# Kernel optimization log

Hardware: AMD Instinct MI355X
Metric: run time of the kernel (lower is better)

## Reference

```python
import jax, jax.numpy as jnp
import numpy as np

N_LAYERS, B, S, D, H, DH = 4, 4, 512, 512, 8, 64
MEM, CMEM, RATIO, FFMUL, VOCAB, LLAT = 512, 128, 4, 4, 512, 256
KV = CMEM + MEM + S  # 1152


def layernorm(x, g, b, eps=1e-5):
    mu = x.mean(-1, keepdims=True)
    var = ((x - mu) ** 2).mean(-1, keepdims=True)
    return (x - mu) * jax.lax.rsqrt(var + eps) * g + b


def shift(x):
    # Music-Transformer skewing: x [..., i, j] -> relative-shifted [..., i, j]
    *lead, i, j = x.shape
    x = jnp.concatenate([x, jnp.zeros((*lead, i, i), x.dtype)], -1)
    l = i + j - 1
    x = x.reshape(*lead, i * (i + j))
    pad = (-x.shape[-1]) % l
    x = jnp.concatenate([x, jnp.zeros((*lead, pad), x.dtype)], -1)
    x = x.reshape(*lead, -1, l)
    return x[..., :i, i - 1:]


def full_attn(q, k, v, mask=None, pos_emb=None):
    dh = q.shape[-1]
    dots = jnp.einsum('bhid,bhjd->bhij', q, k) * (dh ** -0.5)
    if pos_emb is not None:
        pos_dots = jnp.einsum('bhid,hjd->bhij', q, pos_emb) * (dh ** 0.5)
        pos_dots = shift(pos_dots)[..., :dots.shape[-1]]
        dots = dots + pos_dots
    if mask is not None:
        dots = jnp.where(mask, dots, jnp.asarray(-1e9, dots.dtype))
    attn = jax.nn.softmax(dots, -1)
    return jnp.einsum('bhij,bhjd->bhid', attn, v), attn


def heads(x):
    b, n, _ = x.shape
    return x.reshape(b, n, H, DH).transpose(0, 2, 1, 3)


def mha(q_in, k_in, v_in, W, mask=None, pos_emb=None):
    # W: [4, D, D] (q, k, v, out), applied as x @ W
    q, k, v = heads(q_in @ W[0]), heads(k_in @ W[1]), heads(v_in @ W[2])
    x, w = full_attn(q, k, v, mask=mask, pos_emb=pos_emb)
    x = x.transpose(0, 2, 1, 3).reshape(q_in.shape[0], -1, D)
    return x @ W[3], w


def conv_compress(mem, w, b):
    # Conv1d(D, D, RATIO, stride=RATIO): kernel==stride -> block reshape
    Bb, L, _ = mem.shape
    m = mem.reshape(Bb, L // RATIO, RATIO, D)
    return jnp.einsum('blrd,odr->blo', m, w) + b


def forward(trg, trg_mask, src_mask, latent, mems, cmems, pos_emb, embed,
            W_self, ln1_g, ln1_b, conv_w, conv_b, W_src, ln2_g, ln2_b,
            w1, b1, w2, b2):
    x = jnp.take(embed, trg, axis=0)  # [B, S, D]
    tm = trg_mask[:, :, None] & trg_mask[:, None, :]  # [B, S, S]
    tm = jnp.pad(tm, ((0, 0), (0, 0), (CMEM + MEM, 0)), constant_values=True)[:, None]  # [B,1,S,KV]
    sm = src_mask[:, None]  # [B, 1, S, LLAT]
    sg = jax.lax.stop_gradient
    attn_loss = jnp.asarray(0.0, jnp.float32)
    for i in range(N_LAYERS):
        m, cm = mems[i], cmems[i]
        kv = jnp.concatenate([cm, m, x], 1)  # [B, KV, D]
        a, _ = mha(x, kv, kv, W_self[i], mask=tm, pos_emb=pos_emb)
        a = layernorm(a + x, ln1_g[i], ln1_b[i])
        old_mem = m[:, :S]
        new_cm = conv_compress(old_mem, conv_w[i], conv_b[i])  # [B, S//RATIO, D]
        x = a
        # reconstruction attention loss: detached h / weights / old_mem
        Wq, Wk, Wv = sg(W_self[i, 0]), sg(W_self[i, 1]), sg(W_self[i, 2])
        hs = sg(x)

        def rattn(mm):
            q, k, v = heads(hs @ Wq), heads(mm @ Wk), heads(mm @ Wv)
            return full_attn(q, k, v)[0]

        target = sg(rattn(sg(old_mem)))
        attn_loss = attn_loss + jnp.mean((rattn(new_cm) - target) ** 2)
        # cross attention to latent
        x, _ = mha(x, latent, latent, W_src[i], mask=sm)
        # residual pre-norm feed-forward (GELU, exact erf as nn.GELU)
        y = layernorm(x, ln2_g[i], ln2_b[i])
        x = x + jax.nn.gelu(y @ w1[i] + b1[i], approximate=False) @ w2[i] + b2[i]
    return x, attn_loss / N_LAYERS


def setup_inputs() -> dict:
    key = jax.random.key(0)
    ks = jax.random.split(key, 16)
    sc = 0.02
    return {
        'trg': jax.random.randint(ks[0], (B, S), 0, VOCAB, dtype=jnp.int32),
        'trg_mask': jnp.ones((B, S), dtype=bool),
        'src_mask': jnp.ones((B, S, LLAT), dtype=bool),
        'latent': jax.random.normal(ks[1], (B, LLAT, D), jnp.float32),
        'mems': jax.random.normal(ks[2], (N_LAYERS, B, MEM, D), jnp.float32) * sc,
        'cmems': jax.random.normal(ks[3], (N_LAYERS, B, CMEM, D), jnp.float32) * sc,
        'pos_emb': jax.random.normal(ks[4], (H, KV, DH), jnp.float32) * sc,
        'embed': jax.random.normal(ks[5], (VOCAB, D), jnp.float32) * sc,
        'W_self': jax.random.normal(ks[6], (N_LAYERS, 4, D, D), jnp.float32) * sc,
        'ln1_g': jnp.ones((N_LAYERS, D), jnp.float32),
        'ln1_b': jnp.zeros((N_LAYERS, D), jnp.float32),
        'conv_w': jax.random.normal(ks[7], (N_LAYERS, D, D, RATIO), jnp.float32) * sc,
        'conv_b': jnp.zeros((N_LAYERS, D), jnp.float32),
        'W_src': jax.random.normal(ks[8], (N_LAYERS, 4, D, D), jnp.float32) * sc,
        'ln2_g': jnp.ones((N_LAYERS, D), jnp.float32),
        'ln2_b': jnp.zeros((N_LAYERS, D), jnp.float32),
        'w1': jax.random.normal(ks[9], (N_LAYERS, D, D * FFMUL), jnp.float32) * sc,
        'b1': jnp.zeros((N_LAYERS, D * FFMUL), jnp.float32),
        'w2': jax.random.normal(ks[10], (N_LAYERS, D * FFMUL, D), jnp.float32) * sc,
        'b2': jnp.zeros((N_LAYERS, D), jnp.float32),
    }


def reference(trg, trg_mask, src_mask, latent, mems, cmems, pos_emb, embed,
              W_self, ln1_g, ln1_b, conv_w, conv_b, W_src, ln2_g, ln2_b,
              w1, b1, w2, b2):
    return forward(trg, trg_mask, src_mask, latent, mems, cmems, pos_emb, embed,
                   W_self, ln1_g, ln1_b, conv_w, conv_b, W_src, ln2_g, ln2_b,
                   w1, b1, w2, b2)
```

## Files before the change

kernel.cpp:

```cpp
#include <hip/hip_runtime.h>
#include <math.h>

typedef float floatx4 __attribute__((ext_vector_type(4)));
typedef __bf16 bf16x8 __attribute__((ext_vector_type(8)));
typedef unsigned short u16;

#define LDK 72

__device__ inline u16 to_bf16(float f) {
  union { float f; unsigned u; } v; v.f = f;
  unsigned u = v.u;
  u += 0x7FFFu + ((u >> 16) & 1u);
  return (u16)(u >> 16);
}
__device__ inline float bf2f(u16 h) {
  union { unsigned u; float f; } v; v.u = ((unsigned)h) << 16; return v.f;
}

__device__ inline void gload16(const void* g, void* l) {
  __builtin_amdgcn_global_load_lds(
      (const __attribute__((address_space(1))) unsigned int*)g,
      (__attribute__((address_space(3))) unsigned int*)l, 16, 0, 0);
}

struct GemmArgs {
  const void* A; const void* B; void* C;
  int lda, ldb, ldc, N, Kc;
  long sA1, sA2, sB1, sB2, sC1, sC2;
  float alpha;
  const float* bias;
  const float* res; int ldres;
  const float* aml;
  int amode;
  int cmode;
  int act;
  int smode;
  int bdiv, kparts;
  int gx, gy;
};

#define MAXG 6
struct GemmBatch {
  GemmArgs g[MAXG];
  int end[MAXG];
  int ng;
};

__global__ __launch_bounds__(256) void gemmb_k(GemmBatch gb) {
  int bid = blockIdx.x;
  int gi = 0;
  while (bid >= gb.end[gi]) ++gi;
  const GemmArgs g = gb.g[gi];
  int lb = bid - (gi ? gb.end[gi - 1] : 0);
  int bx = lb % g.gx;
  int rem = lb / g.gx;
  int by = rem % g.gy;
  int z = rem / g.gy;

  int kp = z % g.kparts;
  int zz = z / g.kparts;
  int zi = zz / g.bdiv, zj = zz % g.bdiv;
  long aoff = (long)zi * g.sA1 + (long)zj * g.sA2;
  long boff = (long)zi * g.sB1 + (long)zj * g.sB2;
  long coff = (long)zi * g.sC1 + (long)zj * g.sC2;
  const float* Af = (const float*)g.A + aoff;
  const u16* Ah = (const u16*)g.A + aoff;
  const u16* Bh = (const u16*)g.B + boff;

  int m0 = by * 64, n0 = bx * 64;
  __shared__ u16 As[64][64];
  __shared__ u16 Bs[64][64];
  char* Asb = (char*)&As[0][0];
  char* Bsb = (char*)&Bs[0][0];
  int tid = threadIdx.x;
  int wave = tid >> 6, lane = tid & 63;
  int wr = (wave >> 1) * 32, wc = (wave & 1) * 32;
  int lr = lane & 15, qrow = lane >> 4;

  unsigned o0 = wave * 1024u + lane * 16u;
  unsigned o1 = o0 + 4096u;
  int ga_r0 = o0 >> 7, ga_r1 = o1 >> 7;
  int ga_c0 = (int)(o0 & 127u) ^ ((ga_r0 & 7) << 4);
  int ga_c1 = (int)(o1 & 127u) ^ ((ga_r1 & 7) << 4);
  long ldaB = (long)g.lda * 2, ldbB = (long)g.ldb * 2;
  int r = tid >> 2, c16 = (tid & 3) << 4;
  int sw0 = (r << 7) + (((tid & 3) << 5) ^ ((r & 7) << 4));
  int sw1 = (r << 7) + ((((tid & 3) << 5) + 16) ^ ((r & 7) << 4));

  floatx4 acc[2][2];
#pragma unroll
  for (int i = 0; i < 2; ++i)
#pragma unroll
    for (int j = 0; j < 2; ++j)
#pragma unroll
      for (int rr = 0; rr < 4; ++rr) acc[i][j][rr] = 0.f;

  int kb0 = kp * g.Kc, kb1 = kb0 + g.Kc;
  for (int k0 = kb0; k0 < kb1; k0 += 64) {
    if (g.amode == 1) {
      const char* Ab = (const char*)Ah + ((long)m0 * g.lda + k0) * 2;
      gload16(Ab + ga_r0 * ldaB + ga_c0, Asb + wave * 1024);
      gload16(Ab + ga_r1 * ldaB + ga_c1, Asb + 4096 + wave * 1024);
    } else if (g.amode == 0) {
      const float* ap = Af + (long)(m0 + r) * g.lda + k0 + c16;
      float4 a0 = *(const float4*)ap, a1 = *(const float4*)(ap + 4);
      float4 a2 = *(const float4*)(ap + 8), a3 = *(const float4*)(ap + 12);
      union { u16 s[8]; uint4 v; } u0, u1;
      u0.s[0] = to_bf16(a0.x); u0.s[1] = to_bf16(a0.y); u0.s[2] = to_bf16(a0.z); u0.s[3] = to_bf16(a0.w);
      u0.s[4] = to_bf16(a1.x); u0.s[5] = to_bf16(a1.y); u0.s[6] = to_bf16(a1.z); u0.s[7] = to_bf16(a1.w);
      u1.s[0] = to_bf16(a2.x); u1.s[1] = to_bf16(a2.y); u1.s[2] = to_bf16(a2.z); u1.s[3] = to_bf16(a2.w);
      u1.s[4] = to_bf16(a3.x); u1.s[5] = to_bf16(a3.y); u1.s[6] = to_bf16(a3.z); u1.s[7] = to_bf16(a3.w);
      *(uint4*)(Asb + sw0) = u0.v; *(uint4*)(Asb + sw1) = u1.v;
    } else {
      int row = m0 + r;
      int k = k0 + c16;
      const float* mlp = g.aml + ((long)row * 8 + (k >> 6)) * 2;
      float m0v = mlp[0], l0v = mlp[1];
      float m1v = mlp[32768], l1v = mlp[32769];
      float mm = fmaxf(m0v, m1v);
      float w0 = __expf(m0v - mm), w1 = __expf(m1v - mm);
      float inv = 1.f / (w0 * l0v + w1 * l1v);
      w0 *= inv; w1 *= inv;
      const float* p0 = (const float*)g.A + (long)row * g.lda + k;
      const float* p1 = p0 + g.sA1;
      float4 x0 = *(const float4*)p0, x1 = *(const float4*)(p0 + 4);
      float4 x2 = *(const float4*)(p0 + 8), x3 = *(const float4*)(p0 + 12);
      float4 y0 = *(const float4*)p1, y1 = *(const float4*)(p1 + 4);
      float4 y2 = *(const float4*)(p1 + 8), y3 = *(const float4*)(p1 + 12);
      union { u16 s[8]; uint4 v; } u0, u1;
      u0.s[0] = to_bf16(w0 * x0.x + w1 * y0.x); u0.s[1] = to_bf16(w0 * x0.y + w1 * y0.y);
      u0.s[2] = to_bf16(w0 * x0.z + w1 * y0.z); u0.s[3] = to_bf16(w0 * x0.w + w1 * y0.w);
      u0.s[4] = to_bf16(w0 * x1.x + w1 * y1.x); u0.s[5] = to_bf16(w0 * x1.y + w1 * y1.y);
      u0.s[6] = to_bf16(w0 * x1.z + w1 * y1.z); u0.s[7] = to_bf16(w0 * x1.w + w1 * y1.w);
      u1.s[0] = to_bf16(w0 * x2.x + w1 * y2.x); u1.s[1] = to_bf16(w0 * x2.y + w1 * y2.y);
      u1.s[2] = to_bf16(w0 * x2.z + w1 * y2.z); u1.s[3] = to_bf16(w0 * x2.w + w1 * y2.w);
      u1.s[4] = to_bf16(w0 * x3.x + w1 * y3.x); u1.s[5] = to_bf16(w0 * x3.y + w1 * y3.y);
      u1.s[6] = to_bf16(w0 * x3.z + w1 * y3.z); u1.s[7] = to_bf16(w0 * x3.w + w1 * y3.w);
      *(uint4*)(Asb + sw0) = u0.v; *(uint4*)(Asb + sw1) = u1.v;
    }
    {
      const char* Bb = (const char*)Bh + ((long)n0 * g.ldb + k0) * 2;
      gload16(Bb + ga_r0 * ldbB + ga_c0, Bsb + wave * 1024);
      gload16(Bb + ga_r1 * ldbB + ga_c1, Bsb + 4096 + wave * 1024);
    }
    __syncthreads();
#pragma unroll
    for (int ks = 0; ks < 2; ++ks) {
      int xk = ((ks * 32 + qrow * 8) << 1) ^ ((lr & 7) << 4);
      int rA0 = wr + lr, rB0 = wc + lr;
      bf16x8 a0 = *(const bf16x8*)(Asb + (rA0 << 7) + xk);
      bf16x8 a1 = *(const bf16x8*)(Asb + ((rA0 + 16) << 7) + xk);
      bf16x8 b0 = *(const bf16x8*)(Bsb + (rB0 << 7) + xk);
      bf16x8 b1 = *(const bf16x8*)(Bsb + ((rB0 + 16) << 7) + xk);
      acc[0][0] = __builtin_amdgcn_mfma_f32_16x16x32_bf16(a0, b0, acc[0][0], 0, 0, 0);
      acc[0][1] = __builtin_amdgcn_mfma_f32_16x16x32_bf16(a0, b1, acc[0][1], 0, 0, 0);
      acc[1][0] = __builtin_amdgcn_mfma_f32_16x16x32_bf16(a1, b0, acc[1][0], 0, 0, 0);
      acc[1][1] = __builtin_amdgcn_mfma_f32_16x16x32_bf16(a1, b1, acc[1][1], 0, 0, 0);
    }
    __syncthreads();
  }

#pragma unroll
  for (int mt = 0; mt < 2; ++mt)
#pragma unroll
    for (int nt = 0; nt < 2; ++nt) {
      int row0 = m0 + wr + mt * 16 + qrow * 4;
      int col = n0 + wc + nt * 16 + lr;
      if (g.cmode == 2) {
        ushort4 o;
        o.x = to_bf16(acc[mt][nt][0] * g.alpha);
        o.y = to_bf16(acc[mt][nt][1] * g.alpha);
        o.z = to_bf16(acc[mt][nt][2] * g.alpha);
        o.w = to_bf16(acc[mt][nt][3] * g.alpha);
        *(ushort4*)((u16*)g.C + coff + (long)col * g.ldc + row0) = o;
      } else {
#pragma unroll
        for (int rr = 0; rr < 4; ++rr) {
          int row = row0 + rr;
          float v = acc[mt][nt][rr] * g.alpha;
          if (g.cmode == 3) {
            atomicAdd((float*)g.C + coff + (long)row * g.ldc + col, v);
          } else if (g.smode) {
            int oc = col + row - 511;
            if (oc >= 0) ((u16*)g.C + coff)[(long)row * g.ldc + oc] = to_bf16(v);
          } else {
            if (g.bias) v += g.bias[col];
            if (g.res) v += g.res[(long)row * g.ldres + col];
            if (g.act) v = 0.5f * v * (1.0f + erff(v * 0.70710678118654752f));
            if (g.cmode == 1) ((u16*)g.C + coff)[(long)row * g.ldc + col] = to_bf16(v);
            else ((float*)g.C + coff)[(long)row * g.ldc + col] = v;
          }
        }
      }
    }
}

struct FAttnArgs {
  const u16* Q; const u16* K; const u16* V; const u16* QP;
  void* O; float* Opart; float* ml;
  int L, nsplit; long sKb, sVb; int ldV;
  float scale; int obf16;
};

struct FBatch {
  FAttnArgs a[3];
  int zend[3];
  int nf;
};

__global__ __launch_bounds__(256) void fattnb_k(FBatch fb) {
  int zg = blockIdx.z;
  int fi = 0;
  while (zg >= fb.zend[fi]) ++fi;
  const FAttnArgs a = fb.a[fi];
  int zl = zg - (fi ? fb.zend[fi - 1] : 0);

  int qt = blockIdx.x, h = blockIdx.y;
  int b = zl / a.nsplit, sp = zl % a.nsplit;
  int Lc = a.L / a.nsplit, kt0 = sp * Lc, T = Lc >> 6;
  int tid = threadIdx.x, wave = tid >> 6, lane = tid & 63;
// ... 76 lines not shown
        qpr0 = *(const uint4*)(QPr + kt0 + (t + 1) * 64 + qc);
        qpr1 = *(const uint4*)(QPr + kt0 + (t + 1) * 64 + qc + 8);
      }
    } else {
#pragma unroll
      for (int nt = 0; nt < 4; ++nt)
#pragma unroll
        for (int rr = 0; rr < 4; ++rr) sacc[nt][rr] *= a.scale;
    }
#pragma unroll
    for (int rr = 0; rr < 4; ++rr) {
      float m = -1e30f;
#pragma unroll
      for (int nt = 0; nt < 4; ++nt) m = fmaxf(m, sacc[nt][rr]);
      for (int o = 8; o > 0; o >>= 1) m = fmaxf(m, __shfl_xor(m, o, 64));
      float mn = fmaxf(m_run[rr], m);
      float al = __expf(m_run[rr] - mn);
      m_run[rr] = mn;
      float s = 0.f;
#pragma unroll
      for (int nt = 0; nt < 4; ++nt) {
        float p = __expf(sacc[nt][rr] - mn);
        sacc[nt][rr] = p;
        s += p;
      }
      for (int o = 8; o > 0; o >>= 1) s += __shfl_xor(s, o, 64);
      l_run[rr] = l_run[rr] * al + s;
#pragma unroll
      for (int nt = 0; nt < 4; ++nt) oacc[nt][rr] *= al;
    }
#pragma unroll
    for (int nt = 0; nt < 4; ++nt) {
      Ps[wave][quad * 4 + 0][nt * 16 + lr] = to_bf16(sacc[nt][0]);
      Ps[wave][quad * 4 + 1][nt * 16 + lr] = to_bf16(sacc[nt][1]);
      Ps[wave][quad * 4 + 2][nt * 16 + lr] = to_bf16(sacc[nt][2]);
      Ps[wave][quad * 4 + 3][nt * 16 + lr] = to_bf16(sacc[nt][3]);
    }
#pragma unroll
    for (int ks = 0; ks < 2; ++ks) {
      int kq = ks * 32 + quad * 8;
      bf16x8 av = *(const bf16x8*)&Ps[wave][lr][kq];
#pragma unroll
      for (int nt = 0; nt < 4; ++nt) {
        bf16x8 bb = *(const bf16x8*)&Vs[cur][nt * 16 + lr][kq];
        oacc[nt] = __builtin_amdgcn_mfma_f32_16x16x32_bf16(av, bb, oacc[nt], 0, 0, 0);
      }
    }
    if (more) {
      *(uint4*)&Ks[cur ^ 1][r][c] = pk0; *(uint4*)&Ks[cur ^ 1][r][c + 8] = pk1;
      *(uint4*)&Vs[cur ^ 1][r][c] = pv0; *(uint4*)&Vs[cur ^ 1][r][c + 8] = pv1;
    }
  }
  if (a.nsplit == 1) {
    float inv[4];
#pragma unroll
    for (int rr = 0; rr < 4; ++rr) inv[rr] = 1.f / l_run[rr];
#pragma unroll
    for (int nt = 0; nt < 4; ++nt)
#pragma unroll
      for (int rr = 0; rr < 4; ++rr) {
        long row = b * 512 + qt * 64 + wave * 16 + quad * 4 + rr;
        float v = oacc[nt][rr] * inv[rr];
        if (a.obf16) ((u16*)a.O)[row * 512 + h * 64 + nt * 16 + lr] = to_bf16(v);
        else ((float*)a.O)[row * 512 + h * 64 + nt * 16 + lr] = v;
      }
  } else {
#pragma unroll
    for (int nt = 0; nt < 4; ++nt)
#pragma unroll
      for (int rr = 0; rr < 4; ++rr) {
        long row = b * 512 + qt * 64 + wave * 16 + quad * 4 + rr;
        a.Opart[((long)sp * 2048 + row) * 512 + h * 64 + nt * 16 + lr] = oacc[nt][rr];
      }
    if (lr == 0)
#pragma unroll
      for (int rr = 0; rr < 4; ++rr) {
        long row = b * 512 + qt * 64 + wave * 16 + quad * 4 + rr;
        long mi = (((long)sp * 2048 + row) * 8 + h) * 2;
        a.ml[mi] = m_run[rr]; a.ml[mi + 1] = l_run[rr];
      }
  }
}

__global__ __launch_bounds__(256) void embed_k(const int* __restrict__ trg,
                                               const float* __restrict__ embed,
                                               float* __restrict__ x) {
  int i = blockIdx.x * 256 + threadIdx.x;
  int row = i >> 9, d = i & 511;
  x[i] = embed[(long)trg[row] * 512 + d];
}

__global__ __launch_bounds__(256) void concat_kv_k(const float* __restrict__ cmem,
                                                   const float* __restrict__ mem,
                                                   const float* __restrict__ x,
                                                   u16* __restrict__ kv) {
  long i = (long)blockIdx.x * 256 + threadIdx.x;
  int d = i & 511;
  long t = (i >> 9) % 1152;
  long b = (i >> 9) / 1152;
  float v;
  if (t < 128) v = cmem[(b * 128 + t) * 512 + d];
  else if (t < 640) v = mem[(b * 512 + (t - 128)) * 512 + d];
  else v = x[(b * 512 + (t - 640)) * 512 + d];
  kv[i] = to_bf16(v);
}

__global__ __launch_bounds__(256) void layernorm_k(const float* __restrict__ X,
                                                   const float* __restrict__ g,
                                                   const float* __restrict__ b,
                                                   u16* __restrict__ Y) {
  long row = blockIdx.x;
  const float* x = X + row * 512;
  int tid = threadIdx.x;
  float v0 = x[tid], v1 = x[tid + 256];
  __shared__ float red[256];
  red[tid] = v0 + v1; __syncthreads();
  for (int o = 128; o > 0; o >>= 1) { if (tid < o) red[tid] += red[tid + o]; __syncthreads(); }
  float mu = red[0] * (1.f / 512.f);
  __syncthreads();
  float d0 = v0 - mu, d1 = v1 - mu;
  red[tid] = d0 * d0 + d1 * d1; __syncthreads();
  for (int o = 128; o > 0; o >>= 1) { if (tid < o) red[tid] += red[tid + o]; __syncthreads(); }
  float rstd = rsqrtf(red[0] * (1.f / 512.f) + 1e-5f);
  Y[row * 512 + tid] = to_bf16(d0 * rstd * g[tid] + b[tid]);
  Y[row * 512 + tid + 256] = to_bf16(d1 * rstd * g[tid + 256] + b[tid + 256]);
}

__global__ __launch_bounds__(256) void preset_k(float* __restrict__ C,
                                                const float* __restrict__ res,
                                                const float* __restrict__ bias, int nmask) {
  long i = (long)blockIdx.x * 256 + threadIdx.x;
  float v = 0.f;
  if (res) v += res[i];
  if (bias) v += bias[i & nmask];
  C[i] = v;
}

__global__ __launch_bounds__(256) void loss2_k(const float* __restrict__ ocm,
                                               const float* __restrict__ Opart,
                                               const float* __restrict__ ml,
                                               float* __restrict__ acc) {
  float s = 0.f;
  for (long i = (long)blockIdx.x * 256 + threadIdx.x; i < 1048576; i += 256L * 128) {
    int row = (int)(i >> 9), col = (int)(i & 511), h = col >> 6;
    const float* mlp = ml + ((long)row * 8 + h) * 2;
    float m0v = mlp[0], l0v = mlp[1];
    float m1v = mlp[32768], l1v = mlp[32769];
    float mm = fmaxf(m0v, m1v);
    float w0 = __expf(m0v - mm), w1 = __expf(m1v - mm);
    float ov = (w0 * Opart[i] + w1 * Opart[1048576 + i]) / (w0 * l0v + w1 * l1v);
    float d = ocm[i] - ov; s += d * d;
  }
  for (int o = 32; o > 0; o >>= 1) s += __shfl_xor(s, o, 64);
  __shared__ float red[4];
  if ((threadIdx.x & 63) == 0) red[threadIdx.x >> 6] = s;
  __syncthreads();
  if (threadIdx.x == 0) atomicAdd(acc, red[0] + red[1] + red[2] + red[3]);
}

__global__ __launch_bounds__(256) void transpose_bf16_k(const float* __restrict__ in,
                                                        u16* __restrict__ out, int K, int N) {
  long z = blockIdx.z;
  in += z * (long)K * N; out += z * (long)K * N;
  __shared__ float t[32][33];
  int n0 = blockIdx.x * 32, k0 = blockIdx.y * 32;
  int tx = threadIdx.x, ty = threadIdx.y;
  for (int j = 0; j < 32; j += 8) t[ty + j][tx] = in[(long)(k0 + ty + j) * N + n0 + tx];
  __syncthreads();
  for (int j = 0; j < 32; j += 8) out[(long)(n0 + ty + j) * K + k0 + tx] = to_bf16(t[tx][ty + j]);
}

__global__ __launch_bounds__(256) void convw_k(const float* __restrict__ in,
                                               u16* __restrict__ out) {
  int i = blockIdx.x * 256 + threadIdx.x;
  long z = blockIdx.z;
  int o = i >> 11, k = i & 2047;
  int r = k >> 9, d = k & 511;
  out[z * 1048576 + i] = to_bf16(in[z * 1048576 + o * 2048 + d * 4 + r]);
}

__global__ __launch_bounds__(256) void cvt_bf16_k(const float* __restrict__ in,
                                                  u16* __restrict__ out, int n) {
  int i = blockIdx.x * 256 + threadIdx.x;
  if (i < n) out[i] = to_bf16(in[i]);
}

__global__ __launch_bounds__(256) void finalize_k(const float* __restrict__ x,
                                                  const float* __restrict__ loss,
                                                  float* __restrict__ out) {
  long i = (long)blockIdx.x * 256 + threadIdx.x;
  if (i < 1048576) out[i] = x[i];
  else if (i == 1048576) out[i] = loss[0] * (1.f / (1048576.f * 4.f));
}

extern "C" void kernel_launch(void* const* d_in, const int* in_sizes, int n_in,
                              void* d_out, int out_size, void* d_ws, size_t ws_size,
                              hipStream_t stream) {
  (void)in_sizes; (void)n_in; (void)out_size;
  const int* trg = (const int*)d_in[0];
  const float* latent = (const float*)d_in[3];
  const float* mems = (const float*)d_in[4];
  const float* cmems = (const float*)d_in[5];
  const float* pos_emb = (const float*)d_in[6];
  const float* embed = (const float*)d_in[7];
  const float* W_self = (const float*)d_in[8];
  const float* ln1_g = (const float*)d_in[9];
  const float* ln1_b = (const float*)d_in[10];
  const float* conv_w = (const float*)d_in[11];
  const float* conv_b = (const float*)d_in[12];
  const float* W_src = (const float*)d_in[13];
  const float* ln2_g = (const float*)d_in[14];
  const float* ln2_b = (const float*)d_in[15];
  const float* w1 = (const float*)d_in[16];
  const float* b1 = (const float*)d_in[17];
  const float* w2 = (const float*)d_in[18];
  const float* b2 = (const float*)d_in[19];

  float* ws = (float*)d_ws;
  long off = 0;
  auto alloc = [&](long n) { float* p = ws + off; off += (n + 63) & ~63L; return p; };
  float* x    = alloc(1048576);
  float* t0   = alloc(1048576);
  float* t1   = alloc(1048576);
  float* ncm  = alloc(262144);
  float* ocm  = alloc(1048576);
  float* Opart= alloc(2097152);
  u16* h1   = (u16*)Opart;
  float* mlb  = alloc(65536);
  float* Opart2 = alloc(2097152);
  float* mlb2 = alloc(65536);
  u16* qb   = (u16*)alloc(524288);
  u16* qc   = (u16*)alloc(524288);
  u16* xa   = (u16*)alloc(524288);
  u16* t1h  = (u16*)alloc(524288);
  u16* kvcat= (u16*)alloc(1179648);
  u16* kbuf = (u16*)alloc(1179648);
  u16* vbuf = (u16*)alloc(1179648);
  u16* kmem = (u16*)alloc(524288);
  u16* vmem = (u16*)alloc(524288);
  u16* kcm  = (u16*)alloc(131072);
  u16* vcm  = (u16*)alloc(131072);
  u16* klat = (u16*)alloc(262144);
  u16* vlat = (u16*)alloc(262144);
  u16* SQP  = (u16*)alloc(9437184);
  u16* wts  = (u16*)alloc(2097152);
  u16* wsr  = (u16*)alloc(2097152);
  u16* w1t  = (u16*)alloc(2097152);
  u16* w2t  = (u16*)alloc(2097152);
  u16* cwt  = (u16*)alloc(2097152);
  u16* post = (u16*)alloc(294912);
  float* lossacc = alloc(64);
  if ((size_t)off * 4 > ws_size) return;

  hipMemsetAsync(lossacc, 0, 4, stream);
  hipMemsetAsync(SQP, 0, 37748736, stream);
  embed_k<<<4096, 256, 0, stream>>>(trg, embed, x);
  transpose_bf16_k<<<dim3(16, 16, 16), dim3(32, 8), 0, stream>>>(W_self, wts, 512, 512);
  transpose_bf16_k<<<dim3(16, 16, 16), dim3(32, 8), 0, stream>>>(W_src, wsr, 512, 512);
  transpose_bf16_k<<<dim3(64, 16, 4), dim3(32, 8), 0, stream>>>(w1, w1t, 512, 2048);
  transpose_bf16_k<<<dim3(16, 64, 4), dim3(32, 8), 0, stream>>>(w2, w2t, 2048, 512);
  convw_k<<<dim3(4096, 1, 4), 256, 0, stream>>>(conv_w, cwt);
  cvt_bf16_k<<<2304, 256, 0, stream>>>(pos_emb, post, 589824);

  auto ga = []() { GemmArgs g; g.alpha = 1.f; g.bias = nullptr; g.res = nullptr; g.ldres = 512;
                   g.aml = nullptr;
                   g.amode = 0; g.cmode = 0; g.act = 0; g.smode = 0; g.bdiv = 1; g.kparts = 1;
                   g.sA1 = g.sA2 = g.sB1 = g.sB2 = g.sC1 = g.sC2 = 0; g.N = 0;
                   g.gx = g.gy = 1; return g; };
  GemmBatch GB; GB.ng = 0; int gtot = 0;
  auto badd = [&](GemmArgs g, int gx, int gy, int gz) {
    g.gx = gx; g.gy = gy;
    GB.g[GB.ng] = g; gtot += gx * gy * gz; GB.end[GB.ng] = gtot; GB.ng++;
  };
  auto brun = [&]() {
    gemmb_k<<<dim3(gtot), 256, 0, stream>>>(GB);
    GB.ng = 0; gtot = 0;
  };
  auto run1 = [&](GemmArgs g, int gx, int gy, int gz) { badd(g, gx, gy, gz); brun(); };

  FBatch FB; FB.nf = 0; int ztot = 0;
  auto fadd = [&](const u16* Q, const u16* K, const u16* V, const u16* QP, void* O,
                  int L, int nsplit, long sKb, long sVb, int ldV, int obf16,
                  float* Op, float* ml) {
    FAttnArgs a; a.Q = Q; a.K = K; a.V = V; a.QP = QP; a.O = O;
    a.Opart = Op; a.ml = ml;
    a.L = L; a.nsplit = nsplit; a.sKb = sKb; a.sVb = sVb; a.ldV = ldV;
    a.scale = 0.125f; a.obf16 = obf16;
    FB.a[FB.nf] = a; ztot += 4 * nsplit; FB.zend[FB.nf] = ztot; FB.nf++;
  };
  auto frun = [&]() {
    fattnb_k<<<dim3(8, 8, ztot), 256, 0, stream>>>(FB);
    FB.nf = 0; ztot = 0;
  };

  for (int l = 0; l < 4; ++l) {
    const u16* Wt0 = wts + (l * 4 + 0) * 262144;
    const u16* Wt1 = wts + (l * 4 + 1) * 262144;
    const u16* Wt2 = wts + (l * 4 + 2) * 262144;
    const u16* Wt3 = wts + (l * 4 + 3) * 262144;
    const u16* Ws0 = wsr + (l * 4 + 0) * 262144;
    const u16* Ws1 = wsr + (l * 4 + 1) * 262144;
    const u16* Ws2 = wsr + (l * 4 + 2) * 262144;
    const u16* Ws3 = wsr + (l * 4 + 3) * 262144;
    const float* mem_l = mems + (long)l * 1048576;
    const float* cmem_l = cmems + (long)l * 262144;

    concat_kv_k<<<9216, 256, 0, stream>>>(cmem_l, mem_l, x, kvcat);
    preset_k<<<1024, 256, 0, stream>>>(ncm, nullptr, conv_b + l * 512, 511);
    { GemmArgs g = ga(); g.A = x; g.lda = 512; g.B = Wt0; g.ldb = 512; g.C = qb; g.ldc = 512;
      g.cmode = 1; g.Kc = 512; badd(g, 8, 32, 1); }
    { GemmArgs g = ga(); g.A = mem_l; g.lda = 2048; g.B = cwt + (long)l * 1048576; g.ldb = 2048;
      g.C = ncm; g.ldc = 512; g.cmode = 3; g.kparts = 8; g.Kc = 256; badd(g, 8, 8, 8); }
    { GemmArgs g = ga(); g.A = mem_l; g.lda = 512; g.B = Wt1; g.ldb = 512;
      g.C = kmem; g.ldc = 512; g.cmode = 1; g.Kc = 512; badd(g, 8, 32, 1); }
    { GemmArgs g = ga(); g.A = mem_l; g.lda = 512; g.B = Wt2; g.ldb = 512;
      g.C = vmem; g.ldc = 2048; g.cmode = 2; g.Kc = 512; badd(g, 8, 32, 1); }
    { GemmArgs g = ga(); g.A = latent; g.lda = 512; g.B = Ws1; g.ldb = 512;
      g.C = klat; g.ldc = 512; g.cmode = 1; g.Kc = 512; badd(g, 8, 16, 1); }
    { GemmArgs g = ga(); g.A = latent; g.lda = 512; g.B = Ws2; g.ldb = 512;
      g.C = vlat; g.ldc = 1024; g.cmode = 2; g.Kc = 512; badd(g, 8, 16, 1); }
    brun();

    { GemmArgs g = ga(); g.A = kvcat; g.amode = 1; g.lda = 512; g.B = Wt1; g.ldb = 512;
      g.C = kbuf; g.ldc = 512; g.cmode = 1; g.Kc = 512; badd(g, 8, 72, 1); }
    { GemmArgs g = ga(); g.A = kvcat; g.amode = 1; g.lda = 512; g.sA1 = 589824; g.B = Wt2; g.ldb = 512;
      g.C = vbuf; g.ldc = 1152; g.sC1 = 589824; g.cmode = 2; g.Kc = 512; badd(g, 8, 18, 4); }
    { GemmArgs g = ga(); g.A = ncm; g.lda = 512; g.B = Wt1; g.ldb = 512;
      g.C = kcm; g.ldc = 512; g.cmode = 1; g.Kc = 512; badd(g, 8, 8, 1); }
    { GemmArgs g = ga(); g.A = ncm; g.lda = 512; g.B = Wt2; g.ldb = 512;
      g.C = vcm; g.ldc = 512; g.cmode = 2; g.Kc = 512; badd(g, 8, 8, 1); }
    { GemmArgs g = ga(); g.A = qb; g.amode = 1; g.lda = 512; g.sA1 = 262144; g.sA2 = 64;
      g.B = post; g.ldb = 64; g.sB1 = 0; g.sB2 = 73728;
      g.C = SQP; g.ldc = 1152; g.sC1 = 4718592; g.sC2 = 589824;
      g.smode = 1; g.alpha = 8.f; g.bdiv = 8; g.Kc = 64; badd(g, 18, 8, 32); }
    brun();

    fadd(qb, kbuf, vbuf, SQP, nullptr, 1152, 2, 589824, 589824, 1152, 1, Opart, mlb);
    frun();
    { GemmArgs g = ga(); g.A = Opart; g.amode = 2; g.aml = mlb; g.lda = 512; g.sA1 = 1048576;
      g.B = Wt3; g.ldb = 512; g.C = t1; g.ldc = 512; g.res = x; g.Kc = 512; run1(g, 8, 32, 1); }
    layernorm_k<<<2048, 256, 0, stream>>>(t1, ln1_g + l * 512, ln1_b + l * 512, xa);

    { GemmArgs g = ga(); g.A = xa; g.amode = 1; g.lda = 512; g.B = Wt0; g.ldb = 512;
      g.C = qb; g.ldc = 512; g.cmode = 1; g.Kc = 512; badd(g, 8, 32, 1); }
    { GemmArgs g = ga(); g.A = xa; g.amode = 1; g.lda = 512; g.B = Ws0; g.ldb = 512;
      g.C = qc; g.ldc = 512; g.cmode = 1; g.Kc = 512; badd(g, 8, 32, 1); }
    brun();

    fadd(qb, kcm, vcm, nullptr, ocm, 128, 1, 65536, 128, 512, 0, Opart, mlb);
    fadd(qb, kmem, vmem, nullptr, nullptr, 512, 2, 262144, 512, 2048, 0, Opart, mlb);
    fadd(qc, klat, vlat, nullptr, nullptr, 256, 2, 131072, 256, 1024, 1, Opart2, mlb2);
    frun();
    loss2_k<<<128, 256, 0, stream>>>(ocm, Opart, mlb, lossacc);

    { GemmArgs g = ga(); g.A = Opart2; g.amode = 2; g.aml = mlb2; g.lda = 512; g.sA1 = 1048576;
      g.B = Ws3; g.ldb = 512; g.C = t0; g.ldc = 512; g.Kc = 512; run1(g, 8, 32, 1); }
    layernorm_k<<<2048, 256, 0, stream>>>(t0, ln2_g + l * 512, ln2_b + l * 512, t1h);

    { GemmArgs g = ga(); g.A = t1h; g.amode = 1; g.lda = 512; g.B = w1t + (long)l * 1048576; g.ldb = 512;
      g.C = h1; g.ldc = 2048; g.cmode = 1; g.bias = b1 + l * 2048; g.act = 1; g.Kc = 512;
      run1(g, 32, 32, 1); }
    preset_k<<<4096, 256, 0, stream>>>(x, t0, b2 + l * 512, 511);
    { GemmArgs g = ga(); g.A = h1; g.amode = 1; g.lda = 2048; g.B = w2t + (long)l * 1048576; g.ldb = 2048;
      g.C = x; g.ldc = 512; g.cmode = 3; g.kparts = 4; g.Kc = 512; run1(g, 8, 32, 4); }
  }
  finalize_k<<<4097, 256, 0, stream>>>(x, lossacc, (float*)d_out);
}
```

Baseline: 1.161 ms.

## Batch prep kernels, hoist layer-invariant projections, and fold elementwise ops into grouped GEMM launches

All preprocessing kernels (embedding, weight transposes, conv weight reorder, pos_emb conversion, bias preset, memsets) are merged into one batched prep kernel. Latent K/V projections, memory compression and compressed-memory K/V for all layers are hoisted out of the layer loop and computed once. The per-layer bf16 concat buffer is removed by projecting cmem, mem and x directly into kbuf/vbuf. Memory K/V is reused from kbuf/vbuf, and the attention split count goes to 3 with a generalized merge. The loss and residual-preset kernels are folded into the batched GEMM launch as special modes. The aim is fewer launches and less redundant projection work, at the cost of more workspace and a more complex dispatch.

```diff
diff --git a/kernel.cpp b/kernel.cpp
--- a/kernel.cpp
+++ b/kernel.cpp
@@ -39,7 +39,7 @@
   int gx, gy;
 };
 
-#define MAXG 6
+#define MAXG 10
 struct GemmBatch {
   GemmArgs g[MAXG];
   int end[MAXG];
@@ -52,6 +52,42 @@
   while (bid >= gb.end[gi]) ++gi;
   const GemmArgs g = gb.g[gi];
   int lb = bid - (gi ? gb.end[gi - 1] : 0);
+  int tid = threadIdx.x;
+
+  if (g.amode == 8) {
+    long i = (long)lb * 1024 + tid * 4;
+    const float* bs = g.bias;
+    int bi = (int)(i & 511);
+    float4 r = *(const float4*)(g.res + i);
+    float4 v;
+    v.x = r.x + bs[bi]; v.y = r.y + bs[bi + 1];
+    v.z = r.z + bs[bi + 2]; v.w = r.w + bs[bi + 3];
+    *(float4*)((float*)g.C + i) = v;
+    return;
+  }
+  if (g.amode == 9) {
+    const float* oc = (const float*)g.A;
+    const float* Op = (const float*)g.B;
+    const float* ml = g.aml;
+    float s = 0.f;
+    for (long i = (long)lb * 256 + tid; i < 1048576; i += 256L * g.gx) {
+      int row = (int)(i >> 9), col = (int)(i & 511), h = col >> 6;
+      const float* mlp = ml + ((long)row * 8 + h) * 2;
+      float m0v = mlp[0], l0v = mlp[1];
+      float m1v = mlp[32768], l1v = mlp[32769];
+      float mm = fmaxf(m0v, m1v);
+      float w0 = __expf(m0v - mm), w1 = __expf(m1v - mm);
+      float ov = (w0 * Op[i] + w1 * Op[1048576 + i]) / (w0 * l0v + w1 * l1v);
+      float d = oc[i] - ov; s += d * d;
+    }
+    for (int o = 32; o > 0; o >>= 1) s += __shfl_xor(s, o, 64);
+    __shared__ float red[4];
+    if ((tid & 63) == 0) red[tid >> 6] = s;
+    __syncthreads();
+    if (tid == 0) atomicAdd((float*)g.C, red[0] + red[1] + red[2] + red[3]);
+    return;
+  }
+
   int bx = lb % g.gx;
   int rem = lb / g.gx;
   int by = rem % g.gy;
@@ -72,7 +108,6 @@
   __shared__ u16 Bs[64][64];
   char* Asb = (char*)&As[0][0];
   char* Bsb = (char*)&Bs[0][0];
-  int tid = threadIdx.x;
   int wave = tid >> 6, lane = tid & 63;
   int wr = (wave >> 1) * 32, wc = (wave & 1) * 32;
   int lr = lane & 15, qrow = lane >> 4;
@@ -114,28 +149,38 @@
     } else {
       int row = m0 + r;
       int k = k0 + c16;
+      int ns = g.N;
       const float* mlp = g.aml + ((long)row * 8 + (k >> 6)) * 2;
-      float m0v = mlp[0], l0v = mlp[1];
-      float m1v = mlp[32768], l1v = mlp[32769];
-      float mm = fmaxf(m0v, m1v);
-      float w0 = __expf(m0v - mm), w1 = __expf(m1v - mm);
-      float inv = 1.f / (w0 * l0v + w1 * l1v);
-      w0 *= inv; w1 *= inv;
+      float mm = -1e30f;
+#pragma unroll 3
+      for (int s = 0; s < 3; ++s)
+        if (s < ns) mm = fmaxf(mm, mlp[s * 32768]);
+      float wgt[3]; float den = 0.f;
+#pragma unroll 3
+      for (int s = 0; s < 3; ++s)
+        if (s < ns) { wgt[s] = __expf(mlp[s * 32768] - mm); den += wgt[s] * mlp[s * 32768 + 1]; }
+      float inv = 1.f / den;
+      float a16[16];
+#pragma unroll
+      for (int j = 0; j < 16; ++j) a16[j] = 0.f;
       const float* p0 = (const float*)g.A + (long)row * g.lda + k;
-      const float* p1 = p0 + g.sA1;
-      float4 x0 = *(const float4*)p0, x1 = *(const float4*)(p0 + 4);
-      float4 x2 = *(const float4*)(p0 + 8), x3 = *(const float4*)(p0 + 12);
-      float4 y0 = *(const float4*)p1, y1 = *(const float4*)(p1 + 4);
-      float4 y2 = *(const float4*)(p1 + 8), y3 = *(const float4*)(p1 + 12);
+#pragma unroll 3
+      for (int s = 0; s < 3; ++s)
+        if (s < ns) {
+          float w = wgt[s] * inv;
+          const float* p = p0 + (long)s * g.sA1;
+#pragma unroll
+          for (int j = 0; j < 4; ++j) {
+            float4 xx = *(const float4*)(p + j * 4);
+            a16[j * 4 + 0] += w * xx.x; a16[j * 4 + 1] += w * xx.y;
+            a16[j * 4 + 2] += w * xx.z; a16[j * 4 + 3] += w * xx.w;
+          }
+        }
       union { u16 s[8]; uint4 v; } u0, u1;
-      u0.s[0] = to_bf16(w0 * x0.x + w1 * y0.x); u0.s[1] = to_bf16(w0 * x0.y + w1 * y0.y);
-      u0.s[2] = to_bf16(w0 * x0.z + w1 * y0.z); u0.s[3] = to_bf16(w0 * x0.w + w1 * y0.w);
-      u0.s[4] = to_bf16(w0 * x1.x + w1 * y1.x); u0.s[5] = to_bf16(w0 * x1.y + w1 * y1.y);
-      u0.s[6] = to_bf16(w0 * x1.z + w1 * y1.z); u0.s[7] = to_bf16(w0 * x1.w + w1 * y1.w);
-      u1.s[0] = to_bf16(w0 * x2.x + w1 * y2.x); u1.s[1] = to_bf16(w0 * x2.y + w1 * y2.y);
-      u1.s[2] = to_bf16(w0 * x2.z + w1 * y2.z); u1.s[3] = to_bf16(w0 * x2.w + w1 * y2.w);
-      u1.s[4] = to_bf16(w0 * x3.x + w1 * y3.x); u1.s[5] = to_bf16(w0 * x3.y + w1 * y3.y);
-      u1.s[6] = to_bf16(w0 * x3.z + w1 * y3.z); u1.s[7] = to_bf16(w0 * x3.w + w1 * y3.w);
+#pragma unroll
+      for (int j = 0; j < 8; ++j) u0.s[j] = to_bf16(a16[j]);
+#pragma unroll
+      for (int j = 0; j < 8; ++j) u1.s[j] = to_bf16(a16[8 + j]);
       *(uint4*)(Asb + sw0) = u0.v; *(uint4*)(Asb + sw1) = u1.v;
     }
     {
@@ -378,27 +423,45 @@
   }
 }
 
-__global__ __launch_bounds__(256) void embed_k(const int* __restrict__ trg,
-                                               const float* __restrict__ embed,
-                                               float* __restrict__ x) {
-  int i = blockIdx.x * 256 + threadIdx.x;
-  int row = i >> 9, d = i & 511;
-  x[i] = embed[(long)trg[row] * 512 + d];
-}
-
-__global__ __launch_bounds__(256) void concat_kv_k(const float* __restrict__ cmem,
-                                                   const float* __restrict__ mem,
-                                                   const float* __restrict__ x,
-                                                   u16* __restrict__ kv) {
-  long i = (long)blockIdx.x * 256 + threadIdx.x;
-  int d = i & 511;
-  long t = (i >> 9) % 1152;
-  long b = (i >> 9) / 1152;
-  float v;
-  if (t < 128) v = cmem[(b * 128 + t) * 512 + d];
-  else if (t < 640) v = mem[(b * 512 + (t - 128)) * 512 + d];
-  else v = x[(b * 512 + (t - 640)) * 512 + d];
-  kv[i] = to_bf16(v);
+struct PrepArgs { const void* a; const void* b; void* c; int mode, p0, p1, gx, gy; };
+struct PrepBatch { PrepArgs p[10]; int end[10]; int np; };
+
+__global__ __launch_bounds__(256) void prep_k(PrepBatch pb) {
+  int bid = blockIdx.x, gi = 0;
+  while (bid >= pb.end[gi]) ++gi;
+  PrepArgs p = pb.p[gi];
+  int lb = bid - (gi ? pb.end[gi - 1] : 0);
+  int tid = threadIdx.x;
+  __shared__ float t[32][33];
+  if (p.mode == 0) {
+    int i = lb * 256 + tid;
+    int row = i >> 9, d = i & 511;
+    ((float*)p.c)[i] = ((const float*)p.a)[(long)((const int*)p.b)[row] * 512 + d];
+  } else if (p.mode == 1) {
+    int K = p.p0, N = p.p1;
+    int bx = lb % p.gx, by = (lb / p.gx) % p.gy, z = lb / (p.gx * p.gy);
+    const float* in = (const float*)p.a + (long)z * K * N;
+    u16* out = (u16*)p.c + (long)z * K * N;
+    int n0 = bx * 32, k0 = by * 32;
+    int tx = tid & 31, ty = tid >> 5;
+    for (int j = 0; j < 32; j += 8) t[ty + j][tx] = in[(long)(k0 + ty + j) * N + n0 + tx];
+    __syncthreads();
+    for (int j = 0; j < 32; j += 8) out[(long)(n0 + ty + j) * K + k0 + tx] = to_bf16(t[tx][ty + j]);
+  } else if (p.mode == 2) {
+    int z = lb >> 12; int i = (lb & 4095) * 256 + tid;
+    int o = i >> 11, k = i & 2047, r2 = k >> 9, d = k & 511;
+    ((u16*)p.c)[(long)z * 1048576 + i] =
+        to_bf16(((const float*)p.a)[(long)z * 1048576 + o * 2048 + d * 4 + r2]);
+  } else if (p.mode == 3) {
+    int i = lb * 256 + tid;
+    if (i < p.p0) ((u16*)p.c)[i] = to_bf16(((const float*)p.a)[i]);
+  } else if (p.mode == 4) {
+    int i = lb * 256 + tid;
+    ((float*)p.c)[i] = ((const float*)p.a)[((i >> 18) << 9) + (i & 511)];
+  } else {
+    int i = lb * 256 + tid;
+    if (i < p.p0) { uint4 z4 = {0, 0, 0, 0}; ((uint4*)p.c)[i] = z4; }
+  }
 }
 
 __global__ __launch_bounds__(256) void layernorm_k(const float* __restrict__ X,
@@ -420,65 +483,6 @@
   float rstd = rsqrtf(red[0] * (1.f / 512.f) + 1e-5f);
   Y[row * 512 + tid] = to_bf16(d0 * rstd * g[tid] + b[tid]);
   Y[row * 512 + tid + 256] = to_bf16(d1 * rstd * g[tid + 256] + b[tid + 256]);
-}
-
-__global__ __launch_bounds__(256) void preset_k(float* __restrict__ C,
-                                                const float* __restrict__ res,
-                                                const float* __restrict__ bias, int nmask) {
-  long i = (long)blockIdx.x * 256 + threadIdx.x;
-  float v = 0.f;
-  if (res) v += res[i];
-  if (bias) v += bias[i & nmask];
-  C[i] = v;
-}
-
-__global__ __launch_bounds__(256) void loss2_k(const float* __restrict__ ocm,
-                                               const float* __restrict__ Opart,
-                                               const float* __restrict__ ml,
-                                               float* __restrict__ acc) {
-  float s = 0.f;
-  for (long i = (long)blockIdx.x * 256 + threadIdx.x; i < 1048576; i += 256L * 128) {
-    int row = (int)(i >> 9), col = (int)(i & 511), h = col >> 6;
-    const float* mlp = ml + ((long)row * 8 + h) * 2;
-    float m0v = mlp[0], l0v = mlp[1];
-    float m1v = mlp[32768], l1v = mlp[32769];
-    float mm = fmaxf(m0v, m1v);
-    float w0 = __expf(m0v - mm), w1 = __expf(m1v - mm);
-    float ov = (w0 * Opart[i] + w1 * Opart[1048576 + i]) / (w0 * l0v + w1 * l1v);
-    float d = ocm[i] - ov; s += d * d;
-  }
-  for (int o = 32; o > 0; o >>= 1) s += __shfl_xor(s, o, 64);
-  __shared__ float red[4];
-  if ((threadIdx.x & 63) == 0) red[threadIdx.x >> 6] = s;
-  __syncthreads();
-  if (threadIdx.x == 0) atomicAdd(acc, red[0] + red[1] + red[2] + red[3]);
-}
-
-__global__ __launch_bounds__(256) void transpose_bf16_k(const float* __restrict__ in,
-                                                        u16* __restrict__ out, int K, int N) {
-  long z = blockIdx.z;
-  in += z * (long)K * N; out += z * (long)K * N;
-  __shared__ float t[32][33];
-  int n0 = blockIdx.x * 32, k0 = blockIdx.y * 32;
-  int tx = threadIdx.x, ty = threadIdx.y;
-  for (int j = 0; j < 32; j += 8) t[ty + j][tx] = in[(long)(k0 + ty + j) * N + n0 + tx];
-  __syncthreads();
-  for (int j = 0; j < 32; j += 8) out[(long)(n0 + ty + j) * K + k0 + tx] = to_bf16(t[tx][ty + j]);
-}
-
-__global__ __launch_bounds__(256) void convw_k(const float* __restrict__ in,
-                                               u16* __restrict__ out) {
-  int i = blockIdx.x * 256 + threadIdx.x;
-  long z = blockIdx.z;
-  int o = i >> 11, k = i & 2047;
-  int r = k >> 9, d = k & 511;
-  out[z * 1048576 + i] = to_bf16(in[z * 1048576 + o * 2048 + d * 4 + r]);
-}
-
-__global__ __launch_bounds__(256) void cvt_bf16_k(const float* __restrict__ in,
-                                                  u16* __restrict__ out, int n) {
-  int i = blockIdx.x * 256 + threadIdx.x;
-  if (i < n) out[i] = to_bf16(in[i]);
 }
 
 __global__ __launch_bounds__(256) void finalize_k(const float* __restrict__ x,
@@ -518,26 +522,23 @@
   float* x    = alloc(1048576);
   float* t0   = alloc(1048576);
   float* t1   = alloc(1048576);
-  float* ncm  = alloc(262144);
   float* ocm  = alloc(1048576);
-  float* Opart= alloc(2097152);
-  u16* h1   = (u16*)Opart;
-  float* mlb  = alloc(65536);
+  float* Opart= alloc(3145728);
+  float* mlb  = alloc(98304);
   float* Opart2 = alloc(2097152);
+  u16* h1   = (u16*)Opart2;
   float* mlb2 = alloc(65536);
   u16* qb   = (u16*)alloc(524288);
   u16* qc   = (u16*)alloc(524288);
   u16* xa   = (u16*)alloc(524288);
   u16* t1h  = (u16*)alloc(524288);
-  u16* kvcat= (u16*)alloc(1179648);
   u16* kbuf = (u16*)alloc(1179648);
   u16* vbuf = (u16*)alloc(1179648);
-  u16* kmem = (u16*)alloc(524288);
-  u16* vmem = (u16*)alloc(524288);
-  u16* kcm  = (u16*)alloc(131072);
-  u16* vcm  = (u16*)alloc(131072);
-  u16* klat = (u16*)alloc(262144);
-  u16* vlat = (u16*)alloc(262144);
+  u16* kcm4 = (u16*)alloc(524288);
+  u16* vcm4 = (u16*)alloc(524288);
+  u16* klat4= (u16*)alloc(1048576);
+  u16* vlat4= (u16*)alloc(1048576);
+  float* ncm4 = alloc(1048576);
   u16* SQP  = (u16*)alloc(9437184);
   u16* wts  = (u16*)alloc(2097152);
   u16* wsr  = (u16*)alloc(2097152);
@@ -548,15 +549,24 @@
   float* lossacc = alloc(64);
   if ((size_t)off * 4 > ws_size) return;
 
-  hipMemsetAsync(lossacc, 0, 4, stream);
-  hipMemsetAsync(SQP, 0, 37748736, stream);
-  embed_k<<<4096, 256, 0, stream>>>(trg, embed, x);
-  transpose_bf16_k<<<dim3(16, 16, 16), dim3(32, 8), 0, stream>>>(W_self, wts, 512, 512);
-  transpose_bf16_k<<<dim3(16, 16, 16), dim3(32, 8), 0, stream>>>(W_src, wsr, 512, 512);
-  transpose_bf16_k<<<dim3(64, 16, 4), dim3(32, 8), 0, stream>>>(w1, w1t, 512, 2048);
-  transpose_bf16_k<<<dim3(16, 64, 4), dim3(32, 8), 0, stream>>>(w2, w2t, 2048, 512);
-  convw_k<<<dim3(4096, 1, 4), 256, 0, stream>>>(conv_w, cwt);
-  cvt_bf16_k<<<2304, 256, 0, stream>>>(pos_emb, post, 589824);
+  PrepBatch PB; PB.np = 0; int ptot = 0;
+  auto padd = [&](int mode, const void* a, const void* b, void* c,
+                  int p0, int p1, int gx, int gy, int blocks) {
+    PrepArgs pa; pa.a = a; pa.b = b; pa.c = c; pa.mode = mode;
+    pa.p0 = p0; pa.p1 = p1; pa.gx = gx; pa.gy = gy;
+    PB.p[PB.np] = pa; ptot += blocks; PB.end[PB.np] = ptot; PB.np++;
+  };
+  padd(0, embed, trg, x, 0, 0, 0, 0, 4096);
+  padd(1, W_self, nullptr, wts, 512, 512, 16, 16, 4096);
+  padd(1, W_src, nullptr, wsr, 512, 512, 16, 16, 4096);
+  padd(1, w1, nullptr, w1t, 512, 2048, 64, 16, 4096);
+  padd(1, w2, nullptr, w2t, 2048, 512, 16, 64, 4096);
+  padd(2, conv_w, nullptr, cwt, 0, 0, 0, 0, 16384);
+  padd(3, pos_emb, nullptr, post, 589824, 0, 0, 0, 2304);
+  padd(4, conv_b, nullptr, ncm4, 0, 0, 0, 0, 4096);
+  padd(5, nullptr, nullptr, SQP, 2359296, 0, 0, 0, 9216);
+  padd(5, nullptr, nullptr, lossacc, 1, 0, 0, 0, 1);
+  prep_k<<<dim3(ptot), 256, 0, stream>>>(PB);
 
   auto ga = []() { GemmArgs g; g.alpha = 1.f; g.bias = nullptr; g.res = nullptr; g.ldres = 512;
                    g.aml = nullptr;
@@ -589,52 +599,70 @@
     FB.nf = 0; ztot = 0;
   };
 
+  { GemmArgs g = ga(); g.A = latent; g.lda = 512; g.B = wsr + 262144; g.ldb = 512;
+    g.sB1 = 1048576; g.C = klat4; g.ldc = 512; g.sC1 = 524288; g.cmode = 1; g.Kc = 512;
+    badd(g, 8, 16, 4); }
+  { GemmArgs g = ga(); g.A = latent; g.lda = 512; g.B = wsr + 2 * 262144; g.ldb = 512;
+    g.sB1 = 1048576; g.C = vlat4; g.ldc = 1024; g.sC1 = 524288; g.cmode = 2; g.Kc = 512;
+    badd(g, 8, 16, 4); }
+  { GemmArgs g = ga(); g.A = mems; g.lda = 2048; g.sA1 = 1048576;
+    g.B = cwt; g.ldb = 2048; g.sB1 = 1048576;
+    g.C = ncm4; g.ldc = 512; g.sC1 = 262144; g.cmode = 3; g.kparts = 8; g.Kc = 256;
+    badd(g, 8, 8, 32); }
+  brun();
+
   for (int l = 0; l < 4; ++l) {
     const u16* Wt0 = wts + (l * 4 + 0) * 262144;
     const u16* Wt1 = wts + (l * 4 + 1) * 262144;
     const u16* Wt2 = wts + (l * 4 + 2) * 262144;
     const u16* Wt3 = wts + (l * 4 + 3) * 262144;
     const u16* Ws0 = wsr + (l * 4 + 0) * 262144;
-    const u16* Ws1 = wsr + (l * 4 + 1) * 262144;
-    const u16* Ws2 = wsr + (l * 4 + 2) * 262144;
     const u16* Ws3 = wsr + (l * 4 + 3) * 262144;
     const float* mem_l = mems + (long)l * 1048576;
     const float* cmem_l = cmems + (long)l * 262144;
-
-    concat_kv_k<<<9216, 256, 0, stream>>>(cmem_l, mem_l, x, kvcat);
-    preset_k<<<1024, 256, 0, stream>>>(ncm, nullptr, conv_b + l * 512, 511);
+    const u16* kcm_l = kcm4 + (long)l * 262144;
+    const u16* vcm_l = vcm4 + (long)l * 262144;
+    const u16* klat_l = klat4 + (long)l * 524288;
+    const u16* vlat_l = vlat4 + (long)l * 524288;
+
     { GemmArgs g = ga(); g.A = x; g.lda = 512; g.B = Wt0; g.ldb = 512; g.C = qb; g.ldc = 512;
       g.cmode = 1; g.Kc = 512; badd(g, 8, 32, 1); }
-    { GemmArgs g = ga(); g.A = mem_l; g.lda = 2048; g.B = cwt + (long)l * 1048576; g.ldb = 2048;
-      g.C = ncm; g.ldc = 512; g.cmode = 3; g.kparts = 8; g.Kc = 256; badd(g, 8, 8, 8); }
-    { GemmArgs g = ga(); g.A = mem_l; g.lda = 512; g.B = Wt1; g.ldb = 512;
-      g.C = kmem; g.ldc = 512; g.cmode = 1; g.Kc = 512; badd(g, 8, 32, 1); }
-    { GemmArgs g = ga(); g.A = mem_l; g.lda = 512; g.B = Wt2; g.ldb = 512;
-      g.C = vmem; g.ldc = 2048; g.cmode = 2; g.Kc = 512; badd(g, 8, 32, 1); }
-    { GemmArgs g = ga(); g.A = latent; g.lda = 512; g.B = Ws1; g.ldb = 512;
-      g.C = klat; g.ldc = 512; g.cmode = 1; g.Kc = 512; badd(g, 8, 16, 1); }
-    { GemmArgs g = ga(); g.A = latent; g.lda = 512; g.B = Ws2; g.ldb = 512;
-      g.C = vlat; g.ldc = 1024; g.cmode = 2; g.Kc = 512; badd(g, 8, 16, 1); }
+    { GemmArgs g = ga(); g.A = cmem_l; g.lda = 512; g.sA1 = 65536; g.B = Wt1; g.ldb = 512;
+      g.C = kbuf; g.ldc = 512; g.sC1 = 589824; g.cmode = 1; g.Kc = 512; badd(g, 8, 2, 4); }
+    { GemmArgs g = ga(); g.A = mem_l; g.lda = 512; g.sA1 = 262144; g.B = Wt1; g.ldb = 512;
+      g.C = kbuf + 128 * 512; g.ldc = 512; g.sC1 = 589824; g.cmode = 1; g.Kc = 512;
+      badd(g, 8, 8, 4); }
+    { GemmArgs g = ga(); g.A = x; g.lda = 512; g.sA1 = 262144; g.B = Wt1; g.ldb = 512;
+      g.C = kbuf + 640 * 512; g.ldc = 512; g.sC1 = 589824; g.cmode = 1; g.Kc = 512;
+      badd(g, 8, 8, 4); }
+    { GemmArgs g = ga(); g.A = cmem_l; g.lda = 512; g.sA1 = 65536; g.B = Wt2; g.ldb = 512;
+      g.C = vbuf; g.ldc = 1152; g.sC1 = 589824; g.cmode = 2; g.Kc = 512; badd(g, 8, 2, 4); }
+    { GemmArgs g = ga(); g.A = mem_l; g.lda = 512; g.sA1 = 262144; g.B = Wt2; g.ldb = 512;
+      g.C = vbuf + 128; g.ldc = 1152; g.sC1 = 589824; g.cmode = 2; g.Kc = 512;
+      badd(g, 8, 8, 4); }
+    { GemmArgs g = ga(); g.A = x; g.lda = 512; g.sA1 = 262144; g.B = Wt2; g.ldb = 512;
+      g.C = vbuf + 640; g.ldc = 1152; g.sC1 = 589824; g.cmode = 2; g.Kc = 512;
+      badd(g, 8, 8, 4); }
+    if (l == 0) {
+      { GemmArgs g = ga(); g.A = ncm4; g.lda = 512; g.sA1 = 262144; g.B = wts + 262144;
+        g.ldb = 512; g.sB1 = 1048576; g.C = kcm4; g.ldc = 512; g.sC1 = 262144;
+        g.cmode = 1; g.Kc = 512; badd(g, 8, 8, 4); }
+      { GemmArgs g = ga(); g.A = ncm4; g.lda = 512; g.sA1 = 262144; g.B = wts + 2 * 262144;
+        g.ldb = 512; g.sB1 = 1048576; g.C = vcm4; g.ldc = 512; g.sC1 = 262144;
+        g.cmode = 2; g.Kc = 512; badd(g, 8, 8, 4); }
+    }
     brun();
 
-    { GemmArgs g = ga(); g.A = kvcat; g.amode = 1; g.lda = 512; g.B = Wt1; g.ldb = 512;
-      g.C = kbuf; g.ldc = 512; g.cmode = 1; g.Kc = 512; badd(g, 8, 72, 1); }
-    { GemmArgs g = ga(); g.A = kvcat; g.amode = 1; g.lda = 512; g.sA1 = 589824; g.B = Wt2; g.ldb = 512;
-      g.C = vbuf; g.ldc = 1152; g.sC1 = 589824; g.cmode = 2; g.Kc = 512; badd(g, 8, 18, 4); }
-    { GemmArgs g = ga(); g.A = ncm; g.lda = 512; g.B = Wt1; g.ldb = 512;
-      g.C = kcm; g.ldc = 512; g.cmode = 1; g.Kc = 512; badd(g, 8, 8, 1); }
-    { GemmArgs g = ga(); g.A = ncm; g.lda = 512; g.B = Wt2; g.ldb = 512;
-      g.C = vcm; g.ldc = 512; g.cmode = 2; g.Kc = 512; badd(g, 8, 8, 1); }
     { GemmArgs g = ga(); g.A = qb; g.amode = 1; g.lda = 512; g.sA1 = 262144; g.sA2 = 64;
       g.B = post; g.ldb = 64; g.sB1 = 0; g.sB2 = 73728;
       g.C = SQP; g.ldc = 1152; g.sC1 = 4718592; g.sC2 = 589824;
-      g.smode = 1; g.alpha = 8.f; g.bdiv = 8; g.Kc = 64; badd(g, 18, 8, 32); }
-    brun();
-
-    fadd(qb, kbuf, vbuf, SQP, nullptr, 1152, 2, 589824, 589824, 1152, 1, Opart, mlb);
+      g.smode = 1; g.alpha = 8.f; g.bdiv = 8; g.Kc = 64; run1(g, 18, 8, 32); }
+
+    fadd(qb, kbuf, vbuf, SQP, nullptr, 1152, 3, 589824, 589824, 1152, 1, Opart, mlb);
     frun();
-    { GemmArgs g = ga(); g.A = Opart; g.amode = 2; g.aml = mlb; g.lda = 512; g.sA1 = 1048576;
-      g.B = Wt3; g.ldb = 512; g.C = t1; g.ldc = 512; g.res = x; g.Kc = 512; run1(g, 8, 32, 1); }
+    { GemmArgs g = ga(); g.A = Opart; g.amode = 2; g.N = 3; g.aml = mlb; g.lda = 512;
+      g.sA1 = 1048576; g.B = Wt3; g.ldb = 512; g.C = t1; g.ldc = 512; g.res = x; g.Kc = 512;
+      run1(g, 8, 32, 1); }
     layernorm_k<<<2048, 256, 0, stream>>>(t1, ln1_g + l * 512, ln1_b + l * 512, xa);
 
     { GemmArgs g = ga(); g.A = xa; g.amode = 1; g.lda = 512; g.B = Wt0; g.ldb = 512;
@@ -643,22 +671,29 @@
       g.C = qc; g.ldc = 512; g.cmode = 1; g.Kc = 512; badd(g, 8, 32, 1); }
     brun();
 
-    fadd(qb, kcm, vcm, nullptr, ocm, 128, 1, 65536, 128, 512, 0, Opart, mlb);
-    fadd(qb, kmem, vmem, nullptr, nullptr, 512, 2, 262144, 512, 2048, 0, Opart, mlb);
-    fadd(qc, klat, vlat, nullptr, nullptr, 256, 2, 131072, 256, 1024, 1, Opart2, mlb2);
+    fadd(qb, kcm_l, vcm_l, nullptr, ocm, 128, 1, 65536, 128, 512, 0, Opart, mlb);
+    fadd(qb, kbuf + 128 * 512, vbuf + 128, nullptr, nullptr, 512, 2, 589824, 589824, 1152, 0,
+         Opart, mlb);
+    fadd(qc, klat_l, vlat_l, nullptr, nullptr, 256, 2, 131072, 256, 1024, 1, Opart2, mlb2);
     frun();
-    loss2_k<<<128, 256, 0, stream>>>(ocm, Opart, mlb, lossacc);
-
-    { GemmArgs g = ga(); g.A = Opart2; g.amode = 2; g.aml = mlb2; g.lda = 512; g.sA1 = 1048576;
-      g.B = Ws3; g.ldb = 512; g.C = t0; g.ldc = 512; g.Kc = 512; run1(g, 8, 32, 1); }
+
+    { GemmArgs g = ga(); g.A = Opart2; g.amode = 2; g.N = 2; g.aml = mlb2; g.lda = 512;
+      g.sA1 = 1048576; g.B = Ws3; g.ldb = 512; g.C = t0; g.ldc = 512; g.Kc = 512;
+      run1(g, 8, 32, 1); }
     layernorm_k<<<2048, 256, 0, stream>>>(t0, ln2_g + l * 512, ln2_b + l * 512, t1h);
 
-    { GemmArgs g = ga(); g.A = t1h; g.amode = 1; g.lda = 512; g.B = w1t + (long)l * 1048576; g.ldb = 512;
-      g.C = h1; g.ldc = 2048; g.cmode = 1; g.bias = b1 + l * 2048; g.act = 1; g.Kc = 512;
-      run1(g, 32, 32, 1); }
-    preset_k<<<4096, 256, 0, stream>>>(x, t0, b2 + l * 512, 511);
-    { GemmArgs g = ga(); g.A = h1; g.amode = 1; g.lda = 2048; g.B = w2t + (long)l * 1048576; g.ldb = 2048;
-      g.C = x; g.ldc = 512; g.cmode = 3; g.kparts = 4; g.Kc = 512; run1(g, 8, 32, 4); }
+    { GemmArgs g = ga(); g.A = t1h; g.amode = 1; g.lda = 512; g.B = w1t + (long)l * 1048576;
+      g.ldb = 512; g.C = h1; g.ldc = 2048; g.cmode = 1; g.bias = b1 + l * 2048; g.act = 1;
+      g.Kc = 512; badd(g, 32, 32, 1); }
+    { GemmArgs g = ga(); g.amode = 9; g.A = ocm; g.B = Opart; g.aml = mlb; g.C = lossacc;
+      badd(g, 128, 1, 1); }
+    { GemmArgs g = ga(); g.amode = 8; g.res = t0; g.bias = b2 + l * 512; g.C = x;
+      badd(g, 1024, 1, 1); }
+    brun();
+
+    { GemmArgs g = ga(); g.A = h1; g.amode = 1; g.lda = 2048; g.B = w2t + (long)l * 1048576;
+      g.ldb = 2048; g.C = x; g.ldc = 512; g.cmode = 3; g.kparts = 4; g.Kc = 512;
+      run1(g, 8, 32, 4); }
   }
   finalize_k<<<4097, 256, 0, stream>>>(x, lossacc, (float*)d_out);
 }
```

Result: faster. 1.134 ms (-2.3%).
